# Performance work log

Hardware: AMD Instinct MI355X
Metric: run time of the kernel (lower is better)

Reference implementation:

```python
import jax, jax.numpy as jnp
import numpy as np

B, T, D, H, L, R, V = 4, 1024, 1024, 16, 12, 32, 50257
HD = D // H
SCALING = 2.0   # lora_alpha(64) / lora_rank(32) at the default 16-bit precision
EPS = 1e-5
KV_QMAX = float(2 ** 8 - 1)  # kv_cache_bits = 8 (middle of [4,8,16])


def _ln(x, g, b):
    m = jnp.mean(x, -1, keepdims=True)
    v = jnp.mean(jnp.square(x - m), -1, keepdims=True)
    return (x - m) * jax.lax.rsqrt(v + EPS) * g + b


def _round_ste(x):
    return x + jax.lax.stop_gradient(jnp.round(x) - x)


def _fake_quant(x, mn, mx):
    # asymmetric learnable fake-quant with straight-through rounding
    scale = (mx - mn) / KV_QMAX
    zp = _round_ste(-mn / scale)
    q = jnp.clip(_round_ste(x / scale) + zp, 0.0, KV_QMAX)
    return (q - zp) * scale


def _sp_linear(x, w, b, la, lb):
    # quantized-base linear (full precision at 16-bit) + LoRA adapter (eval: no dropout)
    return x @ w + b + SCALING * ((x @ la) @ lb)


def setup_inputs() -> dict:
    key = jax.random.key(0)
    ks = iter(jax.random.split(key, 64))
    rn = lambda shape, s=0.02: jax.random.normal(next(ks), shape, jnp.float32) * s
    return {
        "input_ids": jax.random.randint(next(ks), (B, T), 0, V),
        "wte": rn((V, D)), "wpe": rn((T, D)),
        "ln1_g": jnp.ones((L, D)), "ln1_b": jnp.zeros((L, D)),
        "attn_w": rn((L, D, 3 * D)), "attn_b": jnp.zeros((L, 3 * D)),
        "attn_la": rn((L, D, R)), "attn_lb": rn((L, R, 3 * D)),
        "proj_w": rn((L, D, D)), "proj_b": jnp.zeros((L, D)),
        "proj_la": rn((L, D, R)), "proj_lb": rn((L, R, D)),
        "ln2_g": jnp.ones((L, D)), "ln2_b": jnp.zeros((L, D)),
        "fc_w": rn((L, D, 4 * D)), "fc_b": jnp.zeros((L, 4 * D)),
        "fc_la": rn((L, D, R)), "fc_lb": rn((L, R, 4 * D)),
        "mproj_w": rn((L, 4 * D, D)), "mproj_b": jnp.zeros((L, D)),
        "mproj_la": rn((L, 4 * D, R)), "mproj_lb": rn((L, R, D)),
        "kv_min": jnp.full((L,), -4.0), "kv_max": jnp.full((L,), 4.0),
        "lnf_g": jnp.ones((D,)), "lnf_b": jnp.zeros((D,)),
    }


def reference(input_ids, wte, wpe, ln1_g, ln1_b, attn_w, attn_b, attn_la, attn_lb,
              proj_w, proj_b, proj_la, proj_lb, ln2_g, ln2_b, fc_w, fc_b, fc_la,
              fc_lb, mproj_w, mproj_b, mproj_la, mproj_lb, kv_min, kv_max,
              lnf_g, lnf_b):
    mask = jnp.tril(jnp.ones((T, T), bool))
    h = wte[input_ids] + wpe[None, :T]  # [B,T,D] (dropout is identity in eval)

    def block(h, p):
        (g1, b1, aw, ab, ala, alb, pw, pb, pla, plb, g2, b2,
         fw, fb, fla, flb, mw, mb, mla, mlb, mn, mx) = p
        x = _ln(h, g1, b1)
        qkv = _sp_linear(x, aw, ab, ala, alb)  # [B,T,3D]
        q, k, v = jnp.split(qkv, 3, axis=-1)
        heads = lambda t: t.reshape(B, T, H, HD).transpose(0, 2, 1, 3)  # bhtd
        q, k, v = heads(q), heads(k), heads(v)
        # KV-cache fake quantization (default precision flag unset on attn)
        k = _fake_quant(k, mn, mx)
        v = _fake_quant(v, mn, mx)
        att = jnp.einsum('bhqd,bhkd->bhqk', q, k) / np.float32(np.sqrt(HD))
        att = jax.nn.softmax(jnp.where(mask, att, -jnp.inf), axis=-1)
        o = jnp.einsum('bhqk,bhkd->bhqd', att, v).transpose(0, 2, 1, 3).reshape(B, T, D)
        h = h + _sp_linear(o, pw, pb, pla, plb)
        x = _ln(h, g2, b2)
        m = jax.nn.gelu(_sp_linear(x, fw, fb, fla, flb), approximate=False)
        h = h + _sp_linear(m, mw, mb, mla, mlb)
        return h, None

    params = (ln1_g, ln1_b, attn_w, attn_b, attn_la, attn_lb, proj_w, proj_b,
              proj_la, proj_lb, ln2_g, ln2_b, fc_w, fc_b, fc_la, fc_lb,
              mproj_w, mproj_b, mproj_la, mproj_lb, kv_min, kv_max)
    h, _ = jax.lax.scan(block, h, params)
    return _ln(h, lnf_g, lnf_b)
```

## Files before the change

kernel.cpp:

```cpp
#include <hip/hip_runtime.h>
#include <hip/hip_bf16.h>


typedef __bf16 bf16x8 __attribute__((ext_vector_type(8)));
typedef float f32x4 __attribute__((ext_vector_type(4)));

static __device__ __forceinline__ float bf2f(unsigned short u) {
    union { unsigned int i; float f; } c; c.i = ((unsigned int)u) << 16; return c.f;
}
static __device__ __forceinline__ unsigned short f2bf(float f) {
    unsigned int u = __float_as_uint(f);
    u += 0x7fffu + ((u >> 16) & 1u);
    return (unsigned short)(u >> 16);
}

#define GL2LDS(g, l) __builtin_amdgcn_global_load_lds( \
    (const __attribute__((address_space(1))) unsigned int*)(g), \
    (__attribute__((address_space(3))) unsigned int*)(l), 16, 0, 0)

__global__ __launch_bounds__(256) void k_embed(const int* __restrict__ ids,
        const float* __restrict__ wte, const float* __restrict__ wpe,
        float* __restrict__ h) {
    int row = blockIdx.x;
    int t = row & 1023;
    int id = ids[row];
    int d = threadIdx.x * 4;
    float4 a = *(const float4*)(wte + (size_t)id * 1024 + d);
    float4 b = *(const float4*)(wpe + (size_t)t * 1024 + d);
    float4 o = make_float4(a.x + b.x, a.y + b.y, a.z + b.z, a.w + b.w);
    *(float4*)(h + (size_t)row * 1024 + d) = o;
}

__global__ __launch_bounds__(256) void k_lnf(const float* __restrict__ h,
        const float* __restrict__ g, const float* __restrict__ be,
        float* __restrict__ fo) {
    int row = blockIdx.x, tid = threadIdx.x;
    float4 v = *(const float4*)(h + (size_t)row * 1024 + tid * 4);
    float s = v.x + v.y + v.z + v.w;
    for (int off = 32; off; off >>= 1) s += __shfl_down(s, off);
    __shared__ float red[8];
    int wid = tid >> 6, lane = tid & 63;
    if (!lane) red[wid] = s;
    __syncthreads();
    float mean = (red[0] + red[1] + red[2] + red[3]) * (1.f / 1024.f);
    float dx = v.x - mean, dy = v.y - mean, dz = v.z - mean, dw = v.w - mean;
    float q = dx * dx + dy * dy + dz * dz + dw * dw;
    for (int off = 32; off; off >>= 1) q += __shfl_down(q, off);
    if (!lane) red[4 + wid] = q;
    __syncthreads();
    float var = (red[4] + red[5] + red[6] + red[7]) * (1.f / 1024.f);
    float inv = 1.0f / sqrtf(var + 1e-5f);
    float4 gv = *(const float4*)(g + tid * 4);
    float4 bv = *(const float4*)(be + tid * 4);
    *(float4*)(fo + (size_t)row * 1024 + tid * 4) = make_float4(
        dx * inv * gv.x + bv.x, dy * inv * gv.y + bv.y,
        dz * inv * gv.z + bv.z, dw * inv * gv.w + bv.w);
}

__global__ __launch_bounds__(512) void k_ln_lora(const float* __restrict__ h,
        const float* __restrict__ g, const float* __restrict__ be,
        const unsigned short* __restrict__ laT,
        unsigned short* __restrict__ xo, unsigned short* __restrict__ tmp) {
    __shared__ __align__(16) unsigned short Tx[16][1032];
    __shared__ f32x4 red[2][8][64];
    int tid = threadIdx.x;
    int r = tid >> 5;
    int lr = tid & 31;
    int row = blockIdx.x * 16 + r;
    const float* hrow = h + (size_t)row * 1024;
    float4 xv[8];
    float s = 0.f;
#pragma unroll
    for (int p = 0; p < 8; ++p) {
        xv[p] = *(const float4*)(hrow + p * 128 + lr * 4);
        s += (xv[p].x + xv[p].y) + (xv[p].z + xv[p].w);
    }
    s += __shfl_xor(s, 1); s += __shfl_xor(s, 2); s += __shfl_xor(s, 4);
    s += __shfl_xor(s, 8); s += __shfl_xor(s, 16);
    float mean = s * (1.f / 1024.f);
    float q = 0.f;
#pragma unroll
    for (int p = 0; p < 8; ++p) {
        float a = xv[p].x - mean, b = xv[p].y - mean;
        float c = xv[p].z - mean, d = xv[p].w - mean;
        q += (a * a + b * b) + (c * c + d * d);
    }
    q += __shfl_xor(q, 1); q += __shfl_xor(q, 2); q += __shfl_xor(q, 4);
    q += __shfl_xor(q, 8); q += __shfl_xor(q, 16);
    float inv = 1.0f / sqrtf(q * (1.f / 1024.f) + 1e-5f);
#pragma unroll
    for (int p = 0; p < 8; ++p) {
        int c0 = p * 128 + lr * 4;
        float4 gv = *(const float4*)(g + c0);
        float4 bv = *(const float4*)(be + c0);
        ushort4 o;
        o.x = f2bf((xv[p].x - mean) * inv * gv.x + bv.x);
        o.y = f2bf((xv[p].y - mean) * inv * gv.y + bv.y);
        o.z = f2bf((xv[p].z - mean) * inv * gv.z + bv.z);
        o.w = f2bf((xv[p].w - mean) * inv * gv.w + bv.w);
        *(ushort4*)(xo + (size_t)row * 1024 + c0) = o;
        *(ushort4*)&Tx[r][c0] = o;
    }
    __syncthreads();
    int w = tid >> 6, lane = tid & 63;
    int lrow = lane & 15, lk8 = (lane >> 4) * 8;
    f32x4 acc0 = {0.f, 0.f, 0.f, 0.f}, acc1 = {0.f, 0.f, 0.f, 0.f};
    const unsigned short* b0p = laT + (size_t)lrow * 1024 + w * 128 + lk8;
    const unsigned short* b1p = laT + (size_t)(16 + lrow) * 1024 + w * 128 + lk8;
#pragma unroll
    for (int kt = 0; kt < 128; kt += 32) {
        bf16x8 af = *(const bf16x8*)&Tx[lrow][w * 128 + kt + lk8];
        bf16x8 b0 = *(const bf16x8*)(b0p + kt);
        bf16x8 b1 = *(const bf16x8*)(b1p + kt);
        acc0 = __builtin_amdgcn_mfma_f32_16x16x32_bf16(af, b0, acc0, 0, 0, 0);
        acc1 = __builtin_amdgcn_mfma_f32_16x16x32_bf16(af, b1, acc1, 0, 0, 0);
    }
    red[0][w][lane] = acc0;
    red[1][w][lane] = acc1;
    __syncthreads();
    if (w == 0) {
        acc0 = ((red[0][0][lane] + red[0][1][lane]) + (red[0][2][lane] + red[0][3][lane]))
             + ((red[0][4][lane] + red[0][5][lane]) + (red[0][6][lane] + red[0][7][lane]));
        acc1 = ((red[1][0][lane] + red[1][1][lane]) + (red[1][2][lane] + red[1][3][lane]))
             + ((red[1][4][lane] + red[1][5][lane]) + (red[1][6][lane] + red[1][7][lane]));
        int lq = lane >> 4;
#pragma unroll
        for (int rg = 0; rg < 4; ++rg) {
            int orow = blockIdx.x * 16 + lq * 4 + rg;
            tmp[(size_t)orow * 64 + lrow] = f2bf(acc0[rg]);
            tmp[(size_t)orow * 64 + 16 + lrow] = f2bf(acc1[rg]);
            tmp[(size_t)orow * 64 + 32 + lrow] = 0;
            tmp[(size_t)orow * 64 + 48 + lrow] = 0;
        }
    }
}

__global__ __launch_bounds__(256) void k_lora_mfma(const unsigned short* __restrict__ A,
        const unsigned short* __restrict__ laT, unsigned short* __restrict__ tmp, int K) {
    int rowBase = blockIdx.x * 16;
    int tid = threadIdx.x, w = tid >> 6, lane = tid & 63;
    int lrow = lane & 15, lk8 = (lane >> 4) * 8;
    int kq = K >> 2;
    f32x4 acc0 = {0.f, 0.f, 0.f, 0.f}, acc1 = {0.f, 0.f, 0.f, 0.f};
    const unsigned short* arow = A + (size_t)(rowBase + lrow) * K + w * kq + lk8;
    const unsigned short* b0p = laT + (size_t)lrow * K + w * kq + lk8;
    const unsigned short* b1p = laT + (size_t)(16 + lrow) * K + w * kq + lk8;
#pragma unroll 2
    for (int kt = 0; kt < kq; kt += 32) {
        bf16x8 af = *(const bf16x8*)(arow + kt);
        bf16x8 b0 = *(const bf16x8*)(b0p + kt);
        bf16x8 b1 = *(const bf16x8*)(b1p + kt);
        acc0 = __builtin_amdgcn_mfma_f32_16x16x32_bf16(af, b0, acc0, 0, 0, 0);
        acc1 = __builtin_amdgcn_mfma_f32_16x16x32_bf16(af, b1, acc1, 0, 0, 0);
    }
    __shared__ f32x4 red[2][4][64];
    red[0][w][lane] = acc0;
    red[1][w][lane] = acc1;
    __syncthreads();
    if (w == 0) {
        acc0 = red[0][0][lane] + red[0][1][lane] + red[0][2][lane] + red[0][3][lane];
        acc1 = red[1][0][lane] + red[1][1][lane] + red[1][2][lane] + red[1][3][lane];
        int lq = lane >> 4;
#pragma unroll
        for (int rg = 0; rg < 4; ++rg) {
            int row = rowBase + lq * 4 + rg;
            tmp[(size_t)row * 64 + lrow] = f2bf(acc0[rg]);
            tmp[(size_t)row * 64 + 16 + lrow] = f2bf(acc1[rg]);
            tmp[(size_t)row * 64 + 32 + lrow] = 0;
            tmp[(size_t)row * 64 + 48 + lrow] = 0;
        }
    }
}

__global__ __launch_bounds__(256) void k_prep(
        const float* awB, const float* pwB, const float* fwB, const float* mwB,
        const float* albB, const float* plbB, const float* flbB, const float* mlbB,
        const float* alaB, const float* plaB, const float* flaB, const float* mlaB,
        unsigned short* WTqB, unsigned short* WTpB, unsigned short* WTfB, unsigned short* WTmB,
        unsigned short* LTqB, unsigned short* LTpB, unsigned short* LTfB, unsigned short* LTmB,
        unsigned short* LAqB, unsigned short* LApB, unsigned short* LAfB, unsigned short* LAmB) {
    int bid = blockIdx.x;
    size_t l = blockIdx.y;
    const float* src; unsigned short* dst; int K, N, ntn, local, dstS; float scale = 1.f;
    if      (bid < 768)  { src = awB + l*3145728;  dst = WTqB + l*3145728; K = 1024; N = 3072; ntn = 48; local = bid; dstS = K; }
    else if (bid < 1024) { src = pwB + l*1048576;  dst = WTpB + l*1048576; K = 1024; N = 1024; ntn = 16; local = bid - 768; dstS = K; }
    else if (bid < 2048) { src = fwB + l*4194304;  dst = WTfB + l*4194304; K = 1024; N = 4096; ntn = 64; local = bid - 1024; dstS = K; }
    else if (bid < 3072) { src = mwB + l*4194304;  dst = WTmB + l*4194304; K = 4096; N = 1024; ntn = 16; local = bid - 2048; dstS = K; }
    else if (bid < 3120) { src = albB + l*98304;   dst = LTqB + l*196608;  K = 32;   N = 3072; ntn = 48; local = bid - 3072; scale = 2.f; dstS = 64; }
    else if (bid < 3136) { src = plbB + l*32768;   dst = LTpB + l*65536;   K = 32;   N = 1024; ntn = 16; local = bid - 3120; scale = 2.f; dstS = 64; }
    else if (bid < 3200) { src = flbB + l*131072;  dst = LTfB + l*262144;  K = 32;   N = 4096; ntn = 64; local = bid - 3136; scale = 2.f; dstS = 64; }
    else if (bid < 3216) { src = mlbB + l*32768;   dst = LTmB + l*65536;   K = 32;   N = 1024; ntn = 16; local = bid - 3200; scale = 2.f; dstS = 64; }
    else if (bid < 3232) { src = alaB + l*32768;   dst = LAqB + l*32768;   K = 1024; N = 32;   ntn = 1;  local = bid - 3216; dstS = K; }
    else if (bid < 3248) { src = plaB + l*32768;   dst = LApB + l*32768;   K = 1024; N = 32;   ntn = 1;  local = bid - 3232; dstS = K; }
    else if (bid < 3264) { src = flaB + l*32768;   dst = LAfB + l*32768;   K = 1024; N = 32;   ntn = 1;  local = bid - 3248; dstS = K; }
    else                 { src = mlaB + l*131072;  dst = LAmB + l*131072;  K = 4096; N = 32;   ntn = 1;  local = bid - 3264; dstS = K; }
    int kt = local / ntn, nt = local % ntn;
    int k0 = kt * 64, n0 = nt * 64;
    __shared__ unsigned short Tl[64][66];
    int tid = threadIdx.x;
    int c4 = (tid & 15) * 4;
#pragma unroll
    for (int p = 0; p < 4; ++p) {
        int kl = p * 16 + (tid >> 4);
        if (k0 + kl < K && n0 + c4 < N) {
            float4 v = *(const float4*)(src + (size_t)(k0 + kl) * N + n0 + c4);
            ushort2 o0, o1;
            o0.x = f2bf(v.x * scale); o0.y = f2bf(v.y * scale);
            o1.x = f2bf(v.z * scale); o1.y = f2bf(v.w * scale);
            *(ushort2*)&Tl[kl][c4] = o0;
            *(ushort2*)&Tl[kl][c4 + 2] = o1;
        }
    }
    __syncthreads();
    int nl = tid >> 2;
    int kc = (tid & 3) * 8;
    if (n0 + nl < N) {
#pragma unroll
        for (int hh = 0; hh < 2; ++hh) {
            int kb = kc + hh * 32;
            if (k0 + kb < K) {
                unsigned short pk[8];
#pragma unroll
                for (int j = 0; j < 8; ++j) {
                    pk[j] = Tl[kb + j][nl];
                }
                *(uint4*)(dst + (size_t)(n0 + nl) * dstS + k0 + kb) = *(const uint4*)pk;
            } else if (k0 + kb < dstS) {
                uint4 z; z.x = 0; z.y = 0; z.z = 0; z.w = 0;
                *(uint4*)(dst + (size_t)(n0 + nl) * dstS + k0 + kb) = z;
            }
        }
    }
}

template <int EPI>
__global__ __launch_bounds__(256, 1) void k_gemm128(
        const unsigned short* __restrict__ A, const unsigned short* __restrict__ WT,
        const float* __restrict__ bias, const unsigned short* __restrict__ tmpA,
        const unsigned short* __restrict__ lbT, const float* __restrict__ res,
        float* __restrict__ outF, int N, int K) {
    __shared__ unsigned short lds[9 * 4096];
    const int tid = threadIdx.x;
    const int wid = tid >> 6, lane = tid & 63;
    const int wr = wid >> 1, wc = wid & 1;
    const int nBase = blockIdx.x * 128, rowBase = blockIdx.y * 128;
    const int nk = (K >> 6) + 1;

    f32x4 acc[4][4];
#pragma unroll
    for (int i = 0; i < 4; ++i)
#pragma unroll
        for (int j = 0; j < 4; ++j) acc[i][j] = f32x4{0.f, 0.f, 0.f, 0.f};

    auto stage = [&](int s) {
        int kt = s >> 2, part = s & 3;
        bool dead = kt >= nk;
        unsigned short* dst = &lds[(dead ? 8 : (s & 7)) * 4096];
        bool isA = part >= 2;
        int half = part & 1;
        bool lora = (kt == nk - 1);
#pragma unroll
        for (int i = 0; i < 2; ++i) {
            int o = ((i * 4 + wid) << 10) + (lane << 4);
            int r = o >> 7;
            int col = ((o & 127) ^ (((o >> 9) & 3) << 5)) >> 1;
            const unsigned short* src;
            if (dead) {
                src = A + (lane << 3);
            } else if (isA) {
                int grow = rowBase + half * 64 + r;
                src = lora ? tmpA + (size_t)grow * 64 + col
                           : A + (size_t)grow * K + kt * 64 + col;
            } else {
                int gcol = nBase + half * 64 + r;
                src = lora ? lbT + (size_t)gcol * 64 + col
                           : WT + (size_t)gcol * K + kt * 64 + col;
            }
            GL2LDS(src, dst + ((i * 4 + wid) << 9));
        }
    };

    stage(0); stage(1); stage(2); stage(3);
    stage(4); stage(5); stage(6);
    asm volatile("s_waitcnt vmcnt(6)" ::: "memory");
    __builtin_amdgcn_s_barrier();

    for (int kt = 0; kt < nk; ++kt) {
        const unsigned short* aPart = &lds[(((kt & 1) << 2) + 2 + wr) * 4096];
        const unsigned short* bPart = &lds[(((kt & 1) << 2) + wc) * 4096];
        bf16x8 bfr[4][2];
#pragma unroll
        for (int p = 0; p < 4; ++p) {
            bf16x8 af[2];
#pragma unroll
            for (int kk = 0; kk < 2; ++kk) {
                int row = p * 16 + (lane & 15);
                int cb = (kk * 64 + ((lane >> 4) << 4)) ^ (((row >> 2) & 3) << 5);
                af[kk] = *(const bf16x8*)&aPart[row * 64 + (cb >> 1)];
            }
            if (p == 0) {
#pragma unroll
                for (int n = 0; n < 4; ++n)
#pragma unroll
                    for (int kk = 0; kk < 2; ++kk) {
                        int row = n * 16 + (lane & 15);
                        int cb = (kk * 64 + ((lane >> 4) << 4)) ^ (((row >> 2) & 3) << 5);
                        bfr[n][kk] = *(const bf16x8*)&bPart[row * 64 + (cb >> 1)];
                    }
            }
            stage(p == 0 ? 4 * (kt + 1) + 3 : 4 * (kt + 2) + (p - 1));
            __builtin_amdgcn_s_barrier();
            __builtin_amdgcn_s_setprio(1);
#pragma unroll
            for (int n = 0; n < 4; ++n)
#pragma unroll
                for (int kk = 0; kk < 2; ++kk)
                    acc[p][n] = __builtin_amdgcn_mfma_f32_16x16x32_bf16(
                        af[kk], bfr[n][kk], acc[p][n], 0, 0, 0);
            __builtin_amdgcn_s_setprio(0);
            if (p == 3) asm volatile("s_waitcnt vmcnt(6)" ::: "memory");
            __builtin_amdgcn_s_barrier();
        }
    }

#pragma unroll
    for (int n = 0; n < 4; ++n) {
        int col = nBase + wc * 64 + n * 16 + (lane & 15);
        float bv = bias[col];
#pragma unroll
        for (int m = 0; m < 4; ++m) {
            int row0 = rowBase + wr * 64 + m * 16 + ((lane >> 4) << 2);
#pragma unroll
            for (int rg = 0; rg < 4; ++rg) {
                int row = row0 + rg;
                float v = acc[m][n][rg] + bv;
                size_t idx = (size_t)row * N + col;
                if (EPI == 1) v += res[idx];
                outF[idx] = v;
            }
        }
    }
}

template <int EPI>
__global__ __launch_bounds__(512, 1) void k_gemm256(
        const unsigned short* __restrict__ A, const unsigned short* __restrict__ WT,
        const float* __restrict__ bias, const unsigned short* __restrict__ tmpA,
        const unsigned short* __restrict__ lbT,
        const float* __restrict__ kvmin, const float* __restrict__ kvmax, int layer,
        unsigned short* __restrict__ qh, unsigned short* __restrict__ kh,
        unsigned short* __restrict__ vh,
        float* __restrict__ outF, unsigned short* __restrict__ outH, int N, int K) {
    __shared__ unsigned short lds[9 * 8192];
    const int tid = threadIdx.x;
    const int wid = tid >> 6, lane = tid & 63;
    const int wr = wid >> 2, wc = wid & 3;
    const int nBase = blockIdx.x * 256, rowBase = blockIdx.y * 256;
    const int nk = (K >> 6) + 1;

    f32x4 acc[8][4];
#pragma unroll
    for (int i = 0; i < 8; ++i)
#pragma unroll
        for (int j = 0; j < 4; ++j) acc[i][j] = f32x4{0.f, 0.f, 0.f, 0.f};

    auto stage = [&](int s) {
        int kt = s >> 2, part = s & 3;
        bool dead = kt >= nk;
        unsigned short* dst = &lds[(dead ? 8 : (s & 7)) * 8192];
        bool isA = part >= 2;
        int half = part & 1;
        bool lora = (kt == nk - 1);
#pragma unroll
        for (int i = 0; i < 2; ++i) {
            int o = ((i * 8 + wid) << 10) + (lane << 4);
            int r = o >> 7;
            int col = ((o & 127) ^ (((o >> 9) & 3) << 5)) >> 1;
            const unsigned short* src;
            if (dead) {
                src = A + (lane << 3);
            } else if (isA) {
                int grow = rowBase + half * 128 + r;
                src = lora ? tmpA + (size_t)grow * 64 + col
                           : A + (size_t)grow * K + kt * 64 + col;
            } else {
                int gcol = nBase + half * 128 + r;
                src = lora ? lbT + (size_t)gcol * 64 + col
                           : WT + (size_t)gcol * K + kt * 64 + col;
            }
            GL2LDS(src, dst + ((i * 8 + wid) << 9));
        }
    };

    stage(0); stage(1); stage(2); stage(3);
    stage(4); stage(5); stage(6);
    asm volatile("s_waitcnt vmcnt(6)" ::: "memory");
    __builtin_amdgcn_s_barrier();

    for (int kt = 0; kt < nk; ++kt) {
        const unsigned short* aPart = &lds[(((kt & 1) << 2) + 2 + wr) * 8192];
        const unsigned short* bPart = &lds[(((kt & 1) << 2) + (wc >> 1)) * 8192];
        bf16x8 bfr[4][2];
#pragma unroll
        for (int p = 0; p < 4; ++p) {
            bf16x8 af[2][2];
#pragma unroll
            for (int mm = 0; mm < 2; ++mm)
#pragma unroll
                for (int kk = 0; kk < 2; ++kk) {
                    int row = (p * 2 + mm) * 16 + (lane & 15);
                    int cb = (kk * 64 + ((lane >> 4) << 4)) ^ (((row >> 2) & 3) << 5);
                    af[mm][kk] = *(const bf16x8*)&aPart[row * 64 + (cb >> 1)];
                }
            if (p == 0) {
#pragma unroll
                for (int n = 0; n < 4; ++n)
#pragma unroll
                    for (int kk = 0; kk < 2; ++kk) {
                        int row = ((wc & 1) << 6) + n * 16 + (lane & 15);
                        int cb = (kk * 64 + ((lane >> 4) << 4)) ^ (((row >> 2) & 3) << 5);
                        bfr[n][kk] = *(const bf16x8*)&bPart[row * 64 + (cb >> 1)];
                    }
            }
            stage(p == 0 ? 4 * (kt + 1) + 3 : 4 * (kt + 2) + (p - 1));
            __builtin_amdgcn_s_barrier();
            __builtin_amdgcn_s_setprio(1);
#pragma unroll
            for (int mm = 0; mm < 2; ++mm)
#pragma unroll
                for (int n = 0; n < 4; ++n)
#pragma unroll
                    for (int kk = 0; kk < 2; ++kk)
                        acc[p * 2 + mm][n] = __builtin_amdgcn_mfma_f32_16x16x32_bf16(
                            af[mm][kk], bfr[n][kk], acc[p * 2 + mm][n], 0, 0, 0);
            __builtin_amdgcn_s_setprio(0);
            if (p == 3) asm volatile("s_waitcnt vmcnt(6)" ::: "memory");
            __builtin_amdgcn_s_barrier();
        }
    }

    if (EPI == 3) {
        const int b = rowBase >> 10, t0 = rowBase & 1023;
        const int sec = nBase >> 10, nb = nBase & 1023;
        const int lrow = lane & 15, lq4 = (lane >> 4) << 2;
        float qs = 1.f, qzp = 0.f, qinv = 1.f;
        if (sec) {
            float mnv = kvmin[layer], mxv = kvmax[layer];
            qs = (mxv - mnv) * (1.f / 255.f);
            qzp = rintf(-mnv / qs);
            qinv = 1.f / qs;
        }
#pragma unroll
        for (int n = 0; n < 4; ++n) {
            int dd = wc * 64 + n * 16 + lrow;
            float bv = bias[nBase + dd];
#pragma unroll
            for (int m = 0; m < 8; ++m) {
#pragma unroll
                for (int rg = 0; rg < 4; ++rg) {
                    int tt = wr * 128 + m * 16 + lq4 + rg;
                    float v = acc[m][n][rg] + bv;
                    if (sec) {
                        float qv = rintf(v * qinv) + qzp;
                        qv = fminf(fmaxf(qv, 0.f), 255.f);
                        v = (qv - qzp) * qs;
                    }
                    int r = (sec == 2) ? dd : tt;
                    int c = (sec == 2) ? tt : dd;
                    lds[r * 256 + (c ^ ((r & 7) << 3))] = f2bf(v);
                }
            }
        }
        __syncthreads();
        if (sec < 2) {
            unsigned short* dstp = sec ? kh : qh;
            int tL = tid & 255;
            int hp = tid >> 8;
#pragma unroll
            for (int hi = 0; hi < 2; ++hi) {
                int dL = (hp * 2 + hi) * 64;
                int hh = (nb >> 6) + hp * 2 + hi;
                size_t base = (((size_t)(b * 16 + hh)) * 1024 + t0 + tL) * 64;
#pragma unroll
                for (int j = 0; j < 8; ++j) {
                    int c = (dL + j * 8) ^ ((tL & 7) << 3);
                    *(uint4*)(dstp + base + j * 8) = *(const uint4*)&lds[tL * 256 + c];
                }
            }
        } else {
            int dL = tid & 255;
            int th = (tid >> 8) * 128;
            int hh = (nb >> 6) + (dL >> 6);
            size_t base = (((size_t)(b * 16 + hh)) * 64 + (dL & 63)) * 1024 + t0 + th;
#pragma unroll
            for (int j = 0; j < 16; ++j) {
                int c = (th + j * 8) ^ ((dL & 7) << 3);
                *(uint4*)(vh + base + j * 8) = *(const uint4*)&lds[dL * 256 + c];
            }
        }
    } else {
#pragma unroll
        for (int n = 0; n < 4; ++n) {
            int col = nBase + wc * 64 + n * 16 + (lane & 15);
            float bv = bias[col];
#pragma unroll
            for (int m = 0; m < 8; ++m) {
                int row0 = rowBase + wr * 128 + m * 16 + ((lane >> 4) << 2);
#pragma unroll
                for (int rg = 0; rg < 4; ++rg) {
                    int row = row0 + rg;
                    float v = acc[m][n][rg] + bv;
                    size_t idx = (size_t)row * N + col;
                    v = 0.5f * v * (1.f + erff(v * 0.70710678118654752f));
                    outH[idx] = f2bf(v);
                }
            }
        }
    }
}

__global__ __launch_bounds__(256) void k_attn(const unsigned short* __restrict__ qh,
        const unsigned short* __restrict__ kh, const unsigned short* __restrict__ vh,
        unsigned short* __restrict__ o) {
    int fid = blockIdx.y * 16 + blockIdx.x;
    int wgid = (fid & 7) * 128 + (fid >> 3);
    int bh = wgid >> 4, qb = wgid & 15;
    int b = bh >> 4, hh = bh & 15;
    int tid = threadIdx.x, w = tid >> 6, lane = tid & 63;
    int cq = lane & 15;
    int g = lane >> 4;
    int lk8 = g * 8;
    __shared__ unsigned short Kl[64][72];
    __shared__ unsigned short Vt[64][72];
    __shared__ unsigned short Pl[4][16][72];
    const float SCL = 0.18033688011112042f;
    int qrow = qb * 64 + w * 16 + cq;
    bf16x8 aq[2];
    aq[0] = *(const bf16x8*)(qh + ((size_t)bh * 1024 + qrow) * 64 + lk8);
    aq[1] = *(const bf16x8*)(qh + ((size_t)bh * 1024 + qrow) * 64 + 32 + lk8);
    f32x4 od[4];
#pragma unroll
    for (int i = 0; i < 4; ++i) od[i] = f32x4{0.f, 0.f, 0.f, 0.f};
    float mrun = -3e38f, lrun = 0.f;
    int rl = tid >> 2, seg = (tid & 3) * 16;
    for (int kb = 0; kb <= qb; ++kb) {
        __syncthreads();
        {
            size_t kbase = ((size_t)bh * 1024 + kb * 64 + rl) * 64 + seg;
            *(uint4*)&Kl[rl][seg] = *(const uint4*)(kh + kbase);
            *(uint4*)&Kl[rl][seg + 8] = *(const uint4*)(kh + kbase + 8);
            size_t vbase = ((size_t)bh * 64 + rl) * 1024 + kb * 64 + seg;
            *(uint4*)&Vt[rl][seg] = *(const uint4*)(vh + vbase);
            *(uint4*)&Vt[rl][seg + 8] = *(const uint4*)(vh + vbase + 8);
        }
        __syncthreads();
        f32x4 st[4];
#pragma unroll
        for (int ktile = 0; ktile < 4; ++ktile) {
            f32x4 sacc = f32x4{0.f, 0.f, 0.f, 0.f};
#pragma unroll
            for (int dh = 0; dh < 2; ++dh) {
                bf16x8 bk = *(const bf16x8*)&Kl[ktile * 16 + cq][dh * 32 + lk8];
                sacc = __builtin_amdgcn_mfma_f32_16x16x32_bf16(bk, aq[dh], sacc, 0, 0, 0);
            }
            st[ktile] = sacc * SCL;
        }
        if (kb == qb) {
#pragma unroll
            for (int ktile = 0; ktile < 4; ++ktile) {
#pragma unroll
                for (int rg = 0; rg < 4; ++rg) {
                    int kidx = kb * 64 + ktile * 16 + g * 4 + rg;
                    if (kidx > qrow) st[ktile][rg] = -3e38f;
                }
            }
        }
        float tm[4];
#pragma unroll
        for (int ktile = 0; ktile < 4; ++ktile)
            tm[ktile] = fmaxf(fmaxf(st[ktile][0], st[ktile][1]),
                              fmaxf(st[ktile][2], st[ktile][3]));
        float pmax = fmaxf(fmaxf(tm[0], tm[1]), fmaxf(tm[2], tm[3]));
        pmax = fmaxf(pmax, __shfl_xor(pmax, 16));
        pmax = fmaxf(pmax, __shfl_xor(pmax, 32));
        float mnew = fmaxf(mrun, pmax);
#pragma unroll
        for (int ktile = 0; ktile < 4; ++ktile)
#pragma unroll
            for (int rg = 0; rg < 4; ++rg)
                st[ktile][rg] = exp2f(st[ktile][rg] - mnew);
        float ts[4];
#pragma unroll
        for (int ktile = 0; ktile < 4; ++ktile)
            ts[ktile] = (st[ktile][0] + st[ktile][1]) + (st[ktile][2] + st[ktile][3]);
        float sum = (ts[0] + ts[1]) + (ts[2] + ts[3]);
        sum += __shfl_xor(sum, 16);
        sum += __shfl_xor(sum, 32);
        float corr = exp2f(mrun - mnew);
        lrun = lrun * corr + sum;
        mrun = mnew;
#pragma unroll
        for (int rg = 0; rg < 4; ++rg) {
            float cv = __shfl(corr, (lane & 48) | (g * 4 + rg));
#pragma unroll
            for (int dt = 0; dt < 4; ++dt) od[dt][rg] *= cv;
        }
#pragma unroll
        for (int ktile = 0; ktile < 4; ++ktile) {
            ushort4 pw;
            pw.x = f2bf(st[ktile][0]); pw.y = f2bf(st[ktile][1]);
            pw.z = f2bf(st[ktile][2]); pw.w = f2bf(st[ktile][3]);
            *(ushort4*)&Pl[w][cq][ktile * 16 + g * 4] = pw;
        }
        bf16x8 pa[2];
        pa[0] = *(const bf16x8*)&Pl[w][cq][lk8];
        pa[1] = *(const bf16x8*)&Pl[w][cq][32 + lk8];
#pragma unroll
        for (int dt = 0; dt < 4; ++dt) {
#pragma unroll
            for (int kh2 = 0; kh2 < 2; ++kh2) {
                bf16x8 bv = *(const bf16x8*)&Vt[dt * 16 + cq][kh2 * 32 + lk8];
                od[dt] = __builtin_amdgcn_mfma_f32_16x16x32_bf16(pa[kh2], bv, od[dt], 0, 0, 0);
            }
        }
    }
#pragma unroll
    for (int rg = 0; rg < 4; ++rg) {
        float lv = __shfl(lrun, (lane & 48) | (g * 4 + rg));
        float inv = 1.0f / lv;
        int row = qb * 64 + w * 16 + g * 4 + rg;
#pragma unroll
        for (int dt = 0; dt < 4; ++dt) {
            float val = od[dt][rg] * inv;
            o[((size_t)(b * 1024 + row)) * 1024 + hh * 64 + dt * 16 + cq] = f2bf(val);
        }
    }
}

extern "C" void kernel_launch(void* const* d_in, const int* in_sizes, int n_in,
                              void* d_out, int out_size, void* d_ws, size_t ws_size,
                              hipStream_t stream) {
    const int*   ids      = (const int*)d_in[0];
    const float* wte      = (const float*)d_in[1];
    const float* wpe      = (const float*)d_in[2];
    const float* ln1_g    = (const float*)d_in[3];
    const float* ln1_b    = (const float*)d_in[4];
    const float* attn_w   = (const float*)d_in[5];
    const float* attn_b   = (const float*)d_in[6];
    const float* attn_la  = (const float*)d_in[7];
    const float* attn_lb  = (const float*)d_in[8];
    const float* proj_w   = (const float*)d_in[9];
    const float* proj_b   = (const float*)d_in[10];
    const float* proj_la  = (const float*)d_in[11];
    const float* proj_lb  = (const float*)d_in[12];
    const float* ln2_g    = (const float*)d_in[13];
    const float* ln2_b    = (const float*)d_in[14];
    const float* fc_w     = (const float*)d_in[15];
    const float* fc_b     = (const float*)d_in[16];
    const float* fc_la    = (const float*)d_in[17];
    const float* fc_lb    = (const float*)d_in[18];
    const float* mproj_w  = (const float*)d_in[19];
    const float* mproj_b  = (const float*)d_in[20];
    const float* mproj_la = (const float*)d_in[21];
    const float* mproj_lb = (const float*)d_in[22];
    const float* kv_min   = (const float*)d_in[23];
    const float* kv_max   = (const float*)d_in[24];
    const float* lnf_g    = (const float*)d_in[25];
    const float* lnf_b    = (const float*)d_in[26];

    char* ws = (char*)d_ws;
    size_t off = 0;
    auto alloc = [&](size_t bytes) -> char* {
        char* p = ws + off;
        off = (off + bytes + 255) & ~(size_t)255;
        return p;
    };
    float*          h   = (float*)alloc(4096ull * 1024 * 4);
    unsigned short* xb  = (unsigned short*)alloc(4096ull * 1024 * 2);
    unsigned short* tmp = (unsigned short*)alloc(4096ull * 64 * 2);
    unsigned short* qhb = (unsigned short*)alloc(64ull * 1024 * 64 * 2);
    unsigned short* khb = (unsigned short*)alloc(64ull * 1024 * 64 * 2);
    unsigned short* vhb = (unsigned short*)alloc(64ull * 64 * 1024 * 2);
    unsigned short* ob  = (unsigned short*)alloc(4096ull * 1024 * 2);
    unsigned short* mb  = (unsigned short*)alloc(4096ull * 4096 * 2);
    unsigned short* WTq = (unsigned short*)alloc(12ull * 3072 * 1024 * 2);
    unsigned short* WTp = (unsigned short*)alloc(12ull * 1024 * 1024 * 2);
    unsigned short* WTf = (unsigned short*)alloc(12ull * 4096 * 1024 * 2);
    unsigned short* WTm = (unsigned short*)alloc(12ull * 1024 * 4096 * 2);
    unsigned short* LTq = (unsigned short*)alloc(12ull * 3072 * 64 * 2);
    unsigned short* LTp = (unsigned short*)alloc(12ull * 1024 * 64 * 2);
    unsigned short* LTf = (unsigned short*)alloc(12ull * 4096 * 64 * 2);
    unsigned short* LTm = (unsigned short*)alloc(12ull * 1024 * 64 * 2);
    unsigned short* LAq = (unsigned short*)alloc(12ull * 32 * 1024 * 2);
    unsigned short* LAp = (unsigned short*)alloc(12ull * 32 * 1024 * 2);
    unsigned short* LAf = (unsigned short*)alloc(12ull * 32 * 1024 * 2);
    unsigned short* LAm = (unsigned short*)alloc(12ull * 32 * 4096 * 2);

    k_embed<<<4096, 256, 0, stream>>>(ids, wte, wpe, h);
    k_prep<<<dim3(3328, 12), 256, 0, stream>>>(
        attn_w, proj_w, fc_w, mproj_w,
        attn_lb, proj_lb, fc_lb, mproj_lb,
        attn_la, proj_la, fc_la, mproj_la,
        WTq, WTp, WTf, WTm, LTq, LTp, LTf, LTm, LAq, LAp, LAf, LAm);
    for (int l = 0; l < 12; ++l) {
        k_ln_lora<<<256, 512, 0, stream>>>(h, ln1_g + l * 1024, ln1_b + l * 1024,
                                           LAq + (size_t)l * 32768, xb, tmp);
        k_gemm256<3><<<dim3(12, 16), 512, 0, stream>>>(xb, WTq + (size_t)l * 3145728,
                                                       attn_b + l * 3072, tmp, LTq + (size_t)l * 196608,
                                                       kv_min, kv_max, l, qhb, khb, vhb,
                                                       nullptr, nullptr, 3072, 1024);
        k_attn<<<dim3(16, 64), 256, 0, stream>>>(qhb, khb, vhb, ob);
        k_lora_mfma<<<256, 256, 0, stream>>>(ob, LAp + (size_t)l * 32768, tmp, 1024);
        k_gemm128<1><<<dim3(8, 32), 256, 0, stream>>>(ob, WTp + (size_t)l * 1048576,
                                                      proj_b + l * 1024, tmp, LTp + (size_t)l * 65536,
                                                      h, h, 1024, 1024);
        k_ln_lora<<<256, 512, 0, stream>>>(h, ln2_g + l * 1024, ln2_b + l * 1024,
                                           LAf + (size_t)l * 32768, xb, tmp);
        k_gemm256<2><<<dim3(16, 16), 512, 0, stream>>>(xb, WTf + (size_t)l * 4194304,
                                                       fc_b + l * 4096, tmp, LTf + (size_t)l * 262144,
                                                       nullptr, nullptr, 0, nullptr, nullptr, nullptr,
                                                       nullptr, mb, 4096, 1024);
        k_lora_mfma<<<256, 256, 0, stream>>>(mb, LAm + (size_t)l * 131072, tmp, 4096);
        k_gemm128<1><<<dim3(8, 32), 256, 0, stream>>>(mb, WTm + (size_t)l * 4194304,
                                                      mproj_b + l * 1024, tmp, LTm + (size_t)l * 65536,
                                                      h, h, 1024, 4096);
    }
    k_lnf<<<4096, 256, 0, stream>>>(h, lnf_g, lnf_b, (float*)d_out);
}
```

Before: 3.547 ms.

## Process 128 query rows per attention block to reuse K/V tiles

```diff
diff --git a/kernel.cpp b/kernel.cpp
--- a/kernel.cpp
+++ b/kernel.cpp
@@ -522,9 +522,9 @@
 __global__ __launch_bounds__(256) void k_attn(const unsigned short* __restrict__ qh,
         const unsigned short* __restrict__ kh, const unsigned short* __restrict__ vh,
         unsigned short* __restrict__ o) {
-    int fid = blockIdx.y * 16 + blockIdx.x;
-    int wgid = (fid & 7) * 128 + (fid >> 3);
-    int bh = wgid >> 4, qb = wgid & 15;
+    int fid = blockIdx.y * 8 + blockIdx.x;
+    int wgid = (fid & 7) * 64 + (fid >> 3);
+    int bh = wgid >> 3, qb2 = wgid & 7;
     int b = bh >> 4, hh = bh & 15;
     int tid = threadIdx.x, w = tid >> 6, lane = tid & 63;
     int cq = lane & 15;
@@ -532,18 +532,25 @@
     int lk8 = g * 8;
     __shared__ unsigned short Kl[64][72];
     __shared__ unsigned short Vt[64][72];
-    __shared__ unsigned short Pl[4][16][72];
+    __shared__ unsigned short Pl[4][32][72];
     const float SCL = 0.18033688011112042f;
-    int qrow = qb * 64 + w * 16 + cq;
-    bf16x8 aq[2];
-    aq[0] = *(const bf16x8*)(qh + ((size_t)bh * 1024 + qrow) * 64 + lk8);
-    aq[1] = *(const bf16x8*)(qh + ((size_t)bh * 1024 + qrow) * 64 + 32 + lk8);
-    f32x4 od[4];
-#pragma unroll
-    for (int i = 0; i < 4; ++i) od[i] = f32x4{0.f, 0.f, 0.f, 0.f};
-    float mrun = -3e38f, lrun = 0.f;
+    int qbase = qb2 * 128 + w * 32;
+    bf16x8 aq[2][2];
+#pragma unroll
+    for (int sub = 0; sub < 2; ++sub) {
+        int qrow = qbase + sub * 16 + cq;
+        aq[sub][0] = *(const bf16x8*)(qh + ((size_t)bh * 1024 + qrow) * 64 + lk8);
+        aq[sub][1] = *(const bf16x8*)(qh + ((size_t)bh * 1024 + qrow) * 64 + 32 + lk8);
+    }
+    f32x4 od[2][4];
+#pragma unroll
+    for (int sub = 0; sub < 2; ++sub)
+#pragma unroll
+        for (int i = 0; i < 4; ++i) od[sub][i] = f32x4{0.f, 0.f, 0.f, 0.f};
+    float mrun[2] = {-3e38f, -3e38f}, lrun[2] = {0.f, 0.f};
     int rl = tid >> 2, seg = (tid & 3) * 16;
-    for (int kb = 0; kb <= qb; ++kb) {
+    int kbMax = qb2 * 2 + 1;
+    for (int kb = 0; kb <= kbMax; ++kb) {
         __syncthreads();
         {
             size_t kbase = ((size_t)bh * 1024 + kb * 64 + rl) * 64 + seg;
@@ -554,84 +561,93 @@
             *(uint4*)&Vt[rl][seg + 8] = *(const uint4*)(vh + vbase + 8);
         }
         __syncthreads();
-        f32x4 st[4];
+        f32x4 st[2][4];
 #pragma unroll
         for (int ktile = 0; ktile < 4; ++ktile) {
-            f32x4 sacc = f32x4{0.f, 0.f, 0.f, 0.f};
-#pragma unroll
-            for (int dh = 0; dh < 2; ++dh) {
-                bf16x8 bk = *(const bf16x8*)&Kl[ktile * 16 + cq][dh * 32 + lk8];
-                sacc = __builtin_amdgcn_mfma_f32_16x16x32_bf16(bk, aq[dh], sacc, 0, 0, 0);
-            }
-            st[ktile] = sacc * SCL;
-        }
-        if (kb == qb) {
+            bf16x8 bk0 = *(const bf16x8*)&Kl[ktile * 16 + cq][lk8];
+            bf16x8 bk1 = *(const bf16x8*)&Kl[ktile * 16 + cq][32 + lk8];
+#pragma unroll
+            for (int sub = 0; sub < 2; ++sub) {
+                f32x4 sacc = f32x4{0.f, 0.f, 0.f, 0.f};
+                sacc = __builtin_amdgcn_mfma_f32_16x16x32_bf16(bk0, aq[sub][0], sacc, 0, 0, 0);
+                sacc = __builtin_amdgcn_mfma_f32_16x16x32_bf16(bk1, aq[sub][1], sacc, 0, 0, 0);
+                st[sub][ktile] = sacc * SCL;
+            }
+        }
+#pragma unroll
+        for (int sub = 0; sub < 2; ++sub) {
+            int qrow = qbase + sub * 16 + cq;
+            if (kb * 64 + 63 > qrow) {
+#pragma unroll
+                for (int ktile = 0; ktile < 4; ++ktile)
+#pragma unroll
+                    for (int rg = 0; rg < 4; ++rg) {
+                        int kidx = kb * 64 + ktile * 16 + g * 4 + rg;
+                        if (kidx > qrow) st[sub][ktile][rg] = -3e38f;
+                    }
+            }
+            float tm[4];
+#pragma unroll
+            for (int ktile = 0; ktile < 4; ++ktile)
+                tm[ktile] = fmaxf(fmaxf(st[sub][ktile][0], st[sub][ktile][1]),
+                                  fmaxf(st[sub][ktile][2], st[sub][ktile][3]));
+            float pmax = fmaxf(fmaxf(tm[0], tm[1]), fmaxf(tm[2], tm[3]));
+            pmax = fmaxf(pmax, __shfl_xor(pmax, 16));
+            pmax = fmaxf(pmax, __shfl_xor(pmax, 32));
+            float mnew = fmaxf(mrun[sub], pmax);
+#pragma unroll
+            for (int ktile = 0; ktile < 4; ++ktile)
+#pragma unroll
+                for (int rg = 0; rg < 4; ++rg)
+                    st[sub][ktile][rg] = exp2f(st[sub][ktile][rg] - mnew);
+            float ts[4];
+#pragma unroll
+            for (int ktile = 0; ktile < 4; ++ktile)
+                ts[ktile] = (st[sub][ktile][0] + st[sub][ktile][1])
+                          + (st[sub][ktile][2] + st[sub][ktile][3]);
+            float sum = (ts[0] + ts[1]) + (ts[2] + ts[3]);
+            sum += __shfl_xor(sum, 16);
+            sum += __shfl_xor(sum, 32);
+            float corr = exp2f(mrun[sub] - mnew);
+            lrun[sub] = lrun[sub] * corr + sum;
+            mrun[sub] = mnew;
+#pragma unroll
+            for (int rg = 0; rg < 4; ++rg) {
+                float cv = __shfl(corr, (lane & 48) | (g * 4 + rg));
+#pragma unroll
+                for (int dt = 0; dt < 4; ++dt) od[sub][dt][rg] *= cv;
+            }
 #pragma unroll
             for (int ktile = 0; ktile < 4; ++ktile) {
-#pragma unroll
-                for (int rg = 0; rg < 4; ++rg) {
-                    int kidx = kb * 64 + ktile * 16 + g * 4 + rg;
-                    if (kidx > qrow) st[ktile][rg] = -3e38f;
-                }
-            }
-        }
-        float tm[4];
-#pragma unroll
-        for (int ktile = 0; ktile < 4; ++ktile)
-            tm[ktile] = fmaxf(fmaxf(st[ktile][0], st[ktile][1]),
-                              fmaxf(st[ktile][2], st[ktile][3]));
-        float pmax = fmaxf(fmaxf(tm[0], tm[1]), fmaxf(tm[2], tm[3]));
-        pmax = fmaxf(pmax, __shfl_xor(pmax, 16));
-        pmax = fmaxf(pmax, __shfl_xor(pmax, 32));
-        float mnew = fmaxf(mrun, pmax);
-#pragma unroll
-        for (int ktile = 0; ktile < 4; ++ktile)
-#pragma unroll
-            for (int rg = 0; rg < 4; ++rg)
-                st[ktile][rg] = exp2f(st[ktile][rg] - mnew);
-        float ts[4];
-#pragma unroll
-        for (int ktile = 0; ktile < 4; ++ktile)
-            ts[ktile] = (st[ktile][0] + st[ktile][1]) + (st[ktile][2] + st[ktile][3]);
-        float sum = (ts[0] + ts[1]) + (ts[2] + ts[3]);
-        sum += __shfl_xor(sum, 16);
-        sum += __shfl_xor(sum, 32);
-        float corr = exp2f(mrun - mnew);
-        lrun = lrun * corr + sum;
-        mrun = mnew;
-#pragma unroll
-        for (int rg = 0; rg < 4; ++rg) {
-            float cv = __shfl(corr, (lane & 48) | (g * 4 + rg));
-#pragma unroll
-            for (int dt = 0; dt < 4; ++dt) od[dt][rg] *= cv;
-        }
-#pragma unroll
-        for (int ktile = 0; ktile < 4; ++ktile) {
-            ushort4 pw;
-            pw.x = f2bf(st[ktile][0]); pw.y = f2bf(st[ktile][1]);
-            pw.z = f2bf(st[ktile][2]); pw.w = f2bf(st[ktile][3]);
-            *(ushort4*)&Pl[w][cq][ktile * 16 + g * 4] = pw;
-        }
-        bf16x8 pa[2];
-        pa[0] = *(const bf16x8*)&Pl[w][cq][lk8];
-        pa[1] = *(const bf16x8*)&Pl[w][cq][32 + lk8];
+                ushort4 pw;
+                pw.x = f2bf(st[sub][ktile][0]); pw.y = f2bf(st[sub][ktile][1]);
+                pw.z = f2bf(st[sub][ktile][2]); pw.w = f2bf(st[sub][ktile][3]);
+                *(ushort4*)&Pl[w][sub * 16 + cq][ktile * 16 + g * 4] = pw;
+            }
+        }
 #pragma unroll
         for (int dt = 0; dt < 4; ++dt) {
-#pragma unroll
-            for (int kh2 = 0; kh2 < 2; ++kh2) {
-                bf16x8 bv = *(const bf16x8*)&Vt[dt * 16 + cq][kh2 * 32 + lk8];
-                od[dt] = __builtin_amdgcn_mfma_f32_16x16x32_bf16(pa[kh2], bv, od[dt], 0, 0, 0);
-            }
-        }
-    }
+            bf16x8 bv0 = *(const bf16x8*)&Vt[dt * 16 + cq][lk8];
+            bf16x8 bv1 = *(const bf16x8*)&Vt[dt * 16 + cq][32 + lk8];
+#pragma unroll
+            for (int sub = 0; sub < 2; ++sub) {
+                bf16x8 pa0 = *(const bf16x8*)&Pl[w][sub * 16 + cq][lk8];
+                bf16x8 pa1 = *(const bf16x8*)&Pl[w][sub * 16 + cq][32 + lk8];
+                od[sub][dt] = __builtin_amdgcn_mfma_f32_16x16x32_bf16(pa0, bv0, od[sub][dt], 0, 0, 0);
+                od[sub][dt] = __builtin_amdgcn_mfma_f32_16x16x32_bf16(pa1, bv1, od[sub][dt], 0, 0, 0);
+            }
+        }
+    }
+#pragma unroll
+    for (int sub = 0; sub < 2; ++sub)
 #pragma unroll
     for (int rg = 0; rg < 4; ++rg) {
-        float lv = __shfl(lrun, (lane & 48) | (g * 4 + rg));
+        float lv = __shfl(lrun[sub], (lane & 48) | (g * 4 + rg));
         float inv = 1.0f / lv;
-        int row = qb * 64 + w * 16 + g * 4 + rg;
+        int row = qbase + sub * 16 + g * 4 + rg;
 #pragma unroll
         for (int dt = 0; dt < 4; ++dt) {
-            float val = od[dt][rg] * inv;
+            float val = od[sub][dt][rg] * inv;
             o[((size_t)(b * 1024 + row)) * 1024 + hh * 64 + dt * 16 + cq] = f2bf(val);
         }
     }
@@ -709,7 +725,7 @@
                                                        attn_b + l * 3072, tmp, LTq + (size_t)l * 196608,
                                                        kv_min, kv_max, l, qhb, khb, vhb,
                                                        nullptr, nullptr, 3072, 1024);
-        k_attn<<<dim3(16, 64), 256, 0, stream>>>(qhb, khb, vhb, ob);
+        k_attn<<<dim3(8, 64), 256, 0, stream>>>(qhb, khb, vhb, ob);
         k_lora_mfma<<<256, 256, 0, stream>>>(ob, LAp + (size_t)l * 32768, tmp, 1024);
         k_gemm128<1><<<dim3(8, 32), 256, 0, stream>>>(ob, WTp + (size_t)l * 1048576,
                                                       proj_b + l * 1024, tmp, LTp + (size_t)l * 65536,
```

Measured after the change: 3.704 ms. +4.4%, slower.
